# Performance work log

Measured on AMD Instinct MI355X. Metric: run time of the kernel, lower is better.

## Reference

```python
import jax, jax.numpy as jnp
import numpy as np

D_IN, D_OUT, RANK, N = 4096, 4096, 16, 8192


def _quantize_weight(w, bits):
    # round-to-nearest fake quantization, stored back as floats (as in the torch code)
    absmax = jnp.abs(w).max()
    scale = (2 ** (bits - 1) - 1) / absmax
    q = jnp.clip(jnp.round(w * scale), -2 ** (bits - 1), 2 ** (bits - 1) - 1)
    return q / scale


def _double_quantization(w, bits):
    absmax = jnp.abs(w).max()
    c1 = (2 ** (bits - 1) - 1) / absmax          # scalar fp32 scale
    q = jnp.clip(jnp.round(w * c1), -2 ** (bits - 1), 2 ** (bits - 1) - 1)
    return c1, q / c1                             # c_kbit_2 has same shape as w


def setup_inputs() -> dict:
    key = jax.random.key(0)
    kX, kW, kL1, kL2 = jax.random.split(key, 4)
    X = jax.random.normal(kX, (N, D_IN), dtype=jnp.float32)
    W0 = jax.random.normal(kW, (D_IN, D_OUT), dtype=jnp.float32)
    W_nf4 = _quantize_weight(W0, bits=4)
    c_fp32_1, c_kbit_2 = _double_quantization(W_nf4, bits=8)
    L1 = jax.random.normal(kL1, (D_IN, RANK), dtype=jnp.float32)
    L2 = jax.random.normal(kL2, (RANK, D_OUT), dtype=jnp.float32)
    return {"X": X, "W_nf4": W_nf4, "c_fp32_1": c_fp32_1,
            "c_kbit_2": c_kbit_2, "L1": L1, "L2": L2}


def reference(X, W_nf4, c_fp32_1, c_kbit_2, L1, L2):
    # dequantize: elementwise scalar * elementwise-tensor scaling of stored weight
    W = W_nf4 * c_fp32_1 * c_kbit_2               # [D_IN, D_OUT]
    # main GEMM + low-rank LoRA path, added in the epilogue
    Y = X @ W + (X @ L1) @ L2                     # [N, D_OUT]
    return Y
```

## Files before the change

kernel.cpp:

```cpp
#include <hip/hip_runtime.h>


#define M_ROWS 8192
#define K_DIM  4096
#define N_OUT  4096
#define CVT_BLOCKS 16384
#define PREPW_BLOCKS 4096

typedef float  f32x16 __attribute__((ext_vector_type(16)));
typedef __bf16 bf16x8 __attribute__((ext_vector_type(8)));
typedef unsigned short ushort8v __attribute__((ext_vector_type(8)));

__device__ __forceinline__ unsigned short f2bf(float f) {
    __bf16 h = (__bf16)f;
    union { __bf16 h; unsigned short u; } v; v.h = h;
    return v.u;
}

__global__ __launch_bounds__(256) void prep_kernel(
        const float* __restrict__ X,    ushort8v* __restrict__ Xh,
        const float* __restrict__ Wnf4, const float* __restrict__ c1p,
        const float* __restrict__ c2,   const float* __restrict__ L1,
        const float* __restrict__ L2,   unsigned short* __restrict__ Wt) {
    __shared__ float tile[64][65];
    __shared__ float sL2[16][64];
    __shared__ float sL1[64][16];
    const int t = threadIdx.x;

    if (blockIdx.x < CVT_BLOCKS) {
        size_t tid = (size_t)blockIdx.x * 256 + t;
        const float4* xp = (const float4*)X;
        float4 a = xp[tid * 2];
        float4 b = xp[tid * 2 + 1];
        ushort8v o;
        o[0] = f2bf(a.x); o[1] = f2bf(a.y); o[2] = f2bf(a.z); o[3] = f2bf(a.w);
        o[4] = f2bf(b.x); o[5] = f2bf(b.y); o[6] = f2bf(b.z); o[7] = f2bf(b.w);
        Xh[tid] = o;
        return;
    }

    const int wb = blockIdx.x - CVT_BLOCKS;
    const int n0 = (wb & 63) * 64;
    const int k0 = (wb >> 6) * 64;
    const float c1 = *c1p;

    {
        int r = t >> 4, c4 = (t & 15) * 4;
        *(float4*)&sL2[r][c4] = *(const float4*)&L2[(size_t)r * N_OUT + n0 + c4];
        int r1 = t >> 2, c1v = (t & 3) * 4;
        *(float4*)&sL1[r1][c1v] = *(const float4*)&L1[(size_t)(k0 + r1) * 16 + c1v];
    }
    __syncthreads();

    #pragma unroll
    for (int i = 0; i < 4; ++i) {
        int idx = i * 1024 + t * 4;
        int kk = idx >> 6, nn = idx & 63;
        size_t g = (size_t)(k0 + kk) * N_OUT + n0 + nn;
        float4 w = *(const float4*)&Wnf4[g];
        float4 s = *(const float4*)&c2[g];
        float o0 = w.x * c1 * s.x, o1 = w.y * c1 * s.y;
        float o2 = w.z * c1 * s.z, o3 = w.w * c1 * s.w;
        #pragma unroll
        for (int r = 0; r < 16; ++r) {
            float a = sL1[kk][r];
            o0 += a * sL2[r][nn];     o1 += a * sL2[r][nn + 1];
            o2 += a * sL2[r][nn + 2]; o3 += a * sL2[r][nn + 3];
        }
        tile[kk][nn] = o0; tile[kk][nn + 1] = o1;
        tile[kk][nn + 2] = o2; tile[kk][nn + 3] = o3;
    }
    __syncthreads();

    #pragma unroll
    for (int i = 0; i < 2; ++i) {
        int task = i * 256 + t;
        int kg = task & 7, nn = task >> 3;
        ushort8v o;
        #pragma unroll
        for (int j = 0; j < 8; ++j) o[j] = f2bf(tile[kg * 8 + j][nn]);
        *(ushort8v*)&Wt[(size_t)(n0 + nn) * K_DIM + k0 + kg * 8] = o;
    }
}

__global__ __launch_bounds__(256) void gemm_bt_kernel(
        const __bf16* __restrict__ A, const __bf16* __restrict__ Bt,
        float* __restrict__ C) {
    __shared__ __bf16 As[128 * 32];
    __shared__ __bf16 Bs[128 * 32];

    const int t    = threadIdx.x;
    const int w    = t >> 6;
    const int lane = t & 63;
    const int half = lane >> 5;
    const int l32  = lane & 31;
    const int m0   = blockIdx.y * 128;
    const int n0   = blockIdx.x * 128;
    const int wm   = (w >> 1) * 64;
    const int wn   = (w & 1) * 64;

    const int srow = lane >> 2;
    const int scol = ((lane & 3) ^ ((lane >> 3) & 3)) * 8;
    const int rsw = (l32 >> 1) & 3;

    f32x16 acc[2][2] = {};

    for (int kb = 0; kb < K_DIM; kb += 32) {
        __syncthreads();
        #pragma unroll
        for (int j = 0; j < 2; ++j) {
            int row = w * 32 + j * 16 + srow;
            const __bf16* gp = A + (size_t)(m0 + row) * K_DIM + kb + scol;
            __builtin_amdgcn_global_load_lds(
                (const __attribute__((address_space(1))) unsigned int*)gp,
                (__attribute__((address_space(3))) unsigned int*)(As + (w * 32 + j * 16) * 32),
                16, 0, 0);
        }
        #pragma unroll
        for (int j = 0; j < 2; ++j) {
            int row = w * 32 + j * 16 + srow;
            const __bf16* gp = Bt + (size_t)(n0 + row) * K_DIM + kb + scol;
            __builtin_amdgcn_global_load_lds(
                (const __attribute__((address_space(1))) unsigned int*)gp,
                (__attribute__((address_space(3))) unsigned int*)(Bs + (w * 32 + j * 16) * 32),
                16, 0, 0);
        }
        __syncthreads();

        bf16x8 af[2][2], bf[2][2];
        #pragma unroll
        for (int mt = 0; mt < 2; ++mt)
            #pragma unroll
            for (int ks = 0; ks < 2; ++ks) {
                int row = wm + mt * 32 + l32;
                int slot = (2 * ks + half) ^ rsw;
                af[mt][ks] = *(const bf16x8*)(As + row * 32 + slot * 8);
            }
        #pragma unroll
        for (int nt = 0; nt < 2; ++nt)
            #pragma unroll
            for (int ks = 0; ks < 2; ++ks) {
                int row = wn + nt * 32 + l32;
                int slot = (2 * ks + half) ^ rsw;
                bf[nt][ks] = *(const bf16x8*)(Bs + row * 32 + slot * 8);
            }

        #pragma unroll
        for (int ks = 0; ks < 2; ++ks)
            #pragma unroll
            for (int mt = 0; mt < 2; ++mt)
                #pragma unroll
                for (int nt = 0; nt < 2; ++nt)
                    acc[mt][nt] = __builtin_amdgcn_mfma_f32_32x32x16_bf16(
                        af[mt][ks], bf[nt][ks], acc[mt][nt], 0, 0, 0);
    }

    #pragma unroll
    for (int mt = 0; mt < 2; ++mt)
        #pragma unroll
        for (int nt = 0; nt < 2; ++nt) {
            int col = n0 + wn + nt * 32 + l32;
            #pragma unroll
            for (int reg = 0; reg < 16; ++reg) {
                int row = m0 + wm + mt * 32 + (reg & 3) + 8 * (reg >> 2) + 4 * half;
                C[(size_t)row * N_OUT + col] = acc[mt][nt][reg];
            }
        }
}

extern "C" void kernel_launch(void* const* d_in, const int* in_sizes, int n_in,
                              void* d_out, int out_size, void* d_ws, size_t ws_size,
                              hipStream_t stream) {
    const float* X    = (const float*)d_in[0];
    const float* Wnf4 = (const float*)d_in[1];
    const float* c1   = (const float*)d_in[2];
    const float* c2   = (const float*)d_in[3];
    const float* L1   = (const float*)d_in[4];
    const float* L2   = (const float*)d_in[5];
    float* Y = (float*)d_out;

    unsigned short* Xh = (unsigned short*)d_ws;
    unsigned short* Wt = (unsigned short*)((char*)d_ws + (size_t)M_ROWS * K_DIM * 2);

    prep_kernel<<<CVT_BLOCKS + PREPW_BLOCKS, 256, 0, stream>>>(
        X, (ushort8v*)Xh, Wnf4, c1, c2, L1, L2, Wt);
    gemm_bt_kernel<<<dim3(N_OUT / 128, M_ROWS / 128), 256, 0, stream>>>(
        (const __bf16*)Xh, (const __bf16*)Wt, Y);
}
```

Baseline: 649.4 us.

## Compute LoRA path as separate X@L1 and rank-16 epilogue MFMA instead of folding into W

Previously L1@L2 was folded into the dequantized weight before the bf16 GEMM. Now the prep kernel only dequantizes W with a simpler transpose and no LDS, and also converts L1 and L2 to transposed bf16. A new small MFMA kernel computes T = X@L1 into a global buffer, and the main GEMM adds T@L2 with one extra MFMA step per tile in its epilogue. This removes the rank-16 inner loop from W prep and keeps the LoRA term out of the bf16-rounded weight, at the cost of an extra kernel launch that rereads X (8192x4096 bf16) and a less coalesced W prep pattern.

```diff
diff --git a/kernel.cpp b/kernel.cpp
--- a/kernel.cpp
+++ b/kernel.cpp
@@ -5,11 +5,17 @@
 #define K_DIM  4096
 #define N_OUT  4096
 #define CVT_BLOCKS 16384
-#define PREPW_BLOCKS 4096
+#define WP_BLOCKS  8192
+#define TR_BLOCKS  32
 
 typedef float  f32x16 __attribute__((ext_vector_type(16)));
 typedef __bf16 bf16x8 __attribute__((ext_vector_type(8)));
+typedef float  f32x4  __attribute__((ext_vector_type(4)));
 typedef unsigned short ushort8v __attribute__((ext_vector_type(8)));
+
+__device__ float          Tg[(size_t)M_ROWS * 16];
+__device__ unsigned short L1t[16 * K_DIM];
+__device__ unsigned short L2t[N_OUT * 16];
 
 __device__ __forceinline__ unsigned short f2bf(float f) {
     __bf16 h = (__bf16)f;
@@ -22,9 +28,6 @@
         const float* __restrict__ Wnf4, const float* __restrict__ c1p,
         const float* __restrict__ c2,   const float* __restrict__ L1,
         const float* __restrict__ L2,   unsigned short* __restrict__ Wt) {
-    __shared__ float tile[64][65];
-    __shared__ float sL2[16][64];
-    __shared__ float sL1[64][16];
     const int t = threadIdx.x;
 
     if (blockIdx.x < CVT_BLOCKS) {
@@ -39,48 +42,61 @@
         return;
     }
 
-    const int wb = blockIdx.x - CVT_BLOCKS;
-    const int n0 = (wb & 63) * 64;
-    const int k0 = (wb >> 6) * 64;
-    const float c1 = *c1p;
-
-    {
-        int r = t >> 4, c4 = (t & 15) * 4;
-        *(float4*)&sL2[r][c4] = *(const float4*)&L2[(size_t)r * N_OUT + n0 + c4];
-        int r1 = t >> 2, c1v = (t & 3) * 4;
-        *(float4*)&sL1[r1][c1v] = *(const float4*)&L1[(size_t)(k0 + r1) * 16 + c1v];
-    }
-    __syncthreads();
-
+    if (blockIdx.x < CVT_BLOCKS + WP_BLOCKS) {
+        const int wb = blockIdx.x - CVT_BLOCKS;
+        const int n  = (wb & 63) * 64 + (t & 63);
+        const int k0 = (wb >> 6) * 32 + (t >> 6) * 8;
+        const float c1 = *c1p;
+        ushort8v o;
+        #pragma unroll
+        for (int kk = 0; kk < 8; ++kk) {
+            size_t g = (size_t)(k0 + kk) * N_OUT + n;
+            o[kk] = f2bf(Wnf4[g] * c1 * c2[g]);
+        }
+        *(ushort8v*)&Wt[(size_t)n * K_DIM + k0] = o;
+        return;
+    }
+
+    const int idx = (blockIdx.x - CVT_BLOCKS - WP_BLOCKS) * 256 + t;
+    if (idx < K_DIM) {
+        const float4* lp = (const float4*)&L1[(size_t)idx * 16];
+        float4 r0 = lp[0], r1 = lp[1], r2 = lp[2], r3 = lp[3];
+        float v[16] = {r0.x, r0.y, r0.z, r0.w, r1.x, r1.y, r1.z, r1.w,
+                       r2.x, r2.y, r2.z, r2.w, r3.x, r3.y, r3.z, r3.w};
+        #pragma unroll
+        for (int r = 0; r < 16; ++r)
+            L1t[(size_t)r * K_DIM + idx] = f2bf(v[r]);
+    } else {
+        const int n = idx - K_DIM;
+        ushort8v a, b;
+        #pragma unroll
+        for (int r = 0; r < 8; ++r) a[r] = f2bf(L2[(size_t)r * N_OUT + n]);
+        #pragma unroll
+        for (int r = 0; r < 8; ++r) b[r] = f2bf(L2[(size_t)(r + 8) * N_OUT + n]);
+        *(ushort8v*)&L2t[(size_t)n * 16]     = a;
+        *(ushort8v*)&L2t[(size_t)n * 16 + 8] = b;
+    }
+}
+
+__global__ __launch_bounds__(64) void xl1_kernel(const __bf16* __restrict__ Xh) {
+    const int m0   = blockIdx.x * 16;
+    const int lane = threadIdx.x;
+    const int l15  = lane & 15;
+    const int l4   = lane >> 4;
+
+    const __bf16* ap = Xh + (size_t)(m0 + l15) * K_DIM + l4 * 8;
+    const __bf16* bp = (const __bf16*)L1t + (size_t)l15 * K_DIM + l4 * 8;
+
+    f32x4 acc = {};
+    #pragma unroll 8
+    for (int k = 0; k < K_DIM; k += 32) {
+        bf16x8 af = *(const bf16x8*)(ap + k);
+        bf16x8 bf = *(const bf16x8*)(bp + k);
+        acc = __builtin_amdgcn_mfma_f32_16x16x32_bf16(af, bf, acc, 0, 0, 0);
+    }
     #pragma unroll
-    for (int i = 0; i < 4; ++i) {
-        int idx = i * 1024 + t * 4;
-        int kk = idx >> 6, nn = idx & 63;
-        size_t g = (size_t)(k0 + kk) * N_OUT + n0 + nn;
-        float4 w = *(const float4*)&Wnf4[g];
-        float4 s = *(const float4*)&c2[g];
-        float o0 = w.x * c1 * s.x, o1 = w.y * c1 * s.y;
-        float o2 = w.z * c1 * s.z, o3 = w.w * c1 * s.w;
-        #pragma unroll
-        for (int r = 0; r < 16; ++r) {
-            float a = sL1[kk][r];
-            o0 += a * sL2[r][nn];     o1 += a * sL2[r][nn + 1];
-            o2 += a * sL2[r][nn + 2]; o3 += a * sL2[r][nn + 3];
-        }
-        tile[kk][nn] = o0; tile[kk][nn + 1] = o1;
-        tile[kk][nn + 2] = o2; tile[kk][nn + 3] = o3;
-    }
-    __syncthreads();
-
-    #pragma unroll
-    for (int i = 0; i < 2; ++i) {
-        int task = i * 256 + t;
-        int kg = task & 7, nn = task >> 3;
-        ushort8v o;
-        #pragma unroll
-        for (int j = 0; j < 8; ++j) o[j] = f2bf(tile[kg * 8 + j][nn]);
-        *(ushort8v*)&Wt[(size_t)(n0 + nn) * K_DIM + k0 + kg * 8] = o;
-    }
+    for (int reg = 0; reg < 4; ++reg)
+        Tg[(size_t)(m0 + l4 * 4 + reg) * 16 + l15] = acc[reg];
 }
 
 __global__ __launch_bounds__(256) void gemm_bt_kernel(
@@ -153,6 +169,30 @@
                 for (int nt = 0; nt < 2; ++nt)
                     acc[mt][nt] = __builtin_amdgcn_mfma_f32_32x32x16_bf16(
                         af[mt][ks], bf[nt][ks], acc[mt][nt], 0, 0, 0);
+    }
+
+    {
+        bf16x8 afl[2], bfl[2];
+        #pragma unroll
+        for (int mt = 0; mt < 2; ++mt) {
+            const float* tp = Tg + (size_t)(m0 + wm + mt * 32 + l32) * 16 + half * 8;
+            float4 p0 = *(const float4*)tp;
+            float4 p1 = *(const float4*)(tp + 4);
+            afl[mt][0] = (__bf16)p0.x; afl[mt][1] = (__bf16)p0.y;
+            afl[mt][2] = (__bf16)p0.z; afl[mt][3] = (__bf16)p0.w;
+            afl[mt][4] = (__bf16)p1.x; afl[mt][5] = (__bf16)p1.y;
+            afl[mt][6] = (__bf16)p1.z; afl[mt][7] = (__bf16)p1.w;
+        }
+        #pragma unroll
+        for (int nt = 0; nt < 2; ++nt)
+            bfl[nt] = *(const bf16x8*)((const __bf16*)L2t +
+                        (size_t)(n0 + wn + nt * 32 + l32) * 16 + half * 8);
+        #pragma unroll
+        for (int mt = 0; mt < 2; ++mt)
+            #pragma unroll
+            for (int nt = 0; nt < 2; ++nt)
+                acc[mt][nt] = __builtin_amdgcn_mfma_f32_32x32x16_bf16(
+                    afl[mt], bfl[nt], acc[mt][nt], 0, 0, 0);
     }
 
     #pragma unroll
@@ -182,8 +222,9 @@
     unsigned short* Xh = (unsigned short*)d_ws;
     unsigned short* Wt = (unsigned short*)((char*)d_ws + (size_t)M_ROWS * K_DIM * 2);
 
-    prep_kernel<<<CVT_BLOCKS + PREPW_BLOCKS, 256, 0, stream>>>(
+    prep_kernel<<<CVT_BLOCKS + WP_BLOCKS + TR_BLOCKS, 256, 0, stream>>>(
         X, (ushort8v*)Xh, Wnf4, c1, c2, L1, L2, Wt);
+    xl1_kernel<<<M_ROWS / 16, 64, 0, stream>>>((const __bf16*)Xh);
     gemm_bt_kernel<<<dim3(N_OUT / 128, M_ROWS / 128), 256, 0, stream>>>(
         (const __bf16*)Xh, (const __bf16*)Wt, Y);
 }
```

Result: no change. 649.3 us (-0.0%).
